# Performance work log

Hardware: AMD Instinct MI355X
Metric: run time of the kernel (lower is better)

Reference implementation:

```python
import jax, jax.numpy as jnp
import numpy as np

N, E, D, H, ED = 50000, 150000, 128, 4, 16


def _ln(x, g, b, eps=1e-5):
    m = jnp.mean(x, -1, keepdims=True)
    v = jnp.var(x, -1, keepdims=True)
    return (x - m) / jnp.sqrt(v + eps) * g + b


def _seg_softmax(logits, seg, n):
    # numerically stable softmax over edges grouped by destination node
    m = jax.ops.segment_max(logits, seg, num_segments=n)
    e = jnp.exp(logits - m[seg])
    s = jax.ops.segment_sum(e, seg, num_segments=n)
    return e / (s[seg] + 1e-16)


def setup_inputs():
    key = jax.random.key(0)
    ks = jax.random.split(key, 16)
    def w(i, shape, s=0.05):
        return jax.random.normal(ks[i], shape, jnp.float32) * s
    return dict(
        x=w(0, (N, D), 1.0),
        edge_index=jax.random.randint(ks[1], (2, E), 0, N),
        edge_attr=w(2, (E, ED), 1.0),
        sage_Wl=w(3, (D, D)), sage_Wr=w(4, (D, D)), sage_b=jnp.zeros((D,), jnp.float32),
        tq_W=w(5, (D, H * D)), tq_b=jnp.zeros((H * D,), jnp.float32),
        tk_W=w(6, (D, H * D)), tk_b=jnp.zeros((H * D,), jnp.float32),
        tv_W=w(7, (D, H * D)), tv_b=jnp.zeros((H * D,), jnp.float32),
        te_W=w(8, (ED, H * D)),
        tskip_W=w(9, (D, D)), tskip_b=jnp.zeros((D,), jnp.float32),
        gat_W=w(10, (D, H * D)), gat_att_src=w(11, (H, D)), gat_att_dst=w(12, (H, D)),
        gat_bias=jnp.zeros((D,), jnp.float32),
        gate_short=jnp.ones((1,), jnp.float32), gate_attn=jnp.ones((1,), jnp.float32),
        gate_neighbor=jnp.ones((1,), jnp.float32),
        fus_W=w(13, (3 * D, D)), fus_b=jnp.zeros((D,), jnp.float32),
        fus_g=jnp.ones((D,), jnp.float32), fus_beta=jnp.zeros((D,), jnp.float32),
        norm_g=jnp.ones((D,), jnp.float32), norm_b=jnp.zeros((D,), jnp.float32),
    )


def reference(x, edge_index, edge_attr, sage_Wl, sage_Wr, sage_b,
              tq_W, tq_b, tk_W, tk_b, tv_W, tv_b, te_W, tskip_W, tskip_b,
              gat_W, gat_att_src, gat_att_dst, gat_bias,
              gate_short, gate_attn, gate_neighbor,
              fus_W, fus_b, fus_g, fus_beta, norm_g, norm_b):
    n, d = x.shape
    h = tq_W.shape[1] // d
    src, dst = edge_index[0], edge_index[1]

    # --- SAGEConv: mean aggregation of neighbors + root linear ---
    agg = jax.ops.segment_sum(x[src], dst, num_segments=n)
    cnt = jax.ops.segment_sum(jnp.ones((src.shape[0],), x.dtype), dst, num_segments=n)
    mean = agg / jnp.maximum(cnt, 1.0)[:, None]
    x_short = jax.nn.relu(mean @ sage_Wl + x @ sage_Wr + sage_b)

    # --- TransformerConv (concat=False, edge-conditioned key/value, skip) ---
    q = (x @ tq_W + tq_b).reshape(n, h, d)
    k = (x @ tk_W + tk_b).reshape(n, h, d)
    v = (x @ tv_W + tv_b).reshape(n, h, d)
    e = (edge_attr @ te_W).reshape(-1, h, d)           # [E,H,d]
    logits = jnp.sum(q[dst] * (k[src] + e), -1) / np.float32(np.sqrt(d))  # [E,H]
    alpha = _seg_softmax(logits, dst, n)
    out_t = jax.ops.segment_sum((v[src] + e) * alpha[..., None], dst, num_segments=n).mean(1)
    x_attn = jax.nn.relu(out_t + x @ tskip_W + tskip_b)

    # --- GATConv (adds self-loops, concat=False averages heads, bias) ---
    loops = jnp.arange(n)
    s2 = jnp.concatenate([src, loops])
    d2 = jnp.concatenate([dst, loops])
    g = (x @ gat_W).reshape(n, h, d)
    a_s = jnp.sum(g * gat_att_src, -1)                 # [N,H]
    a_d = jnp.sum(g * gat_att_dst, -1)
    lg = jax.nn.leaky_relu(a_s[s2] + a_d[d2], 0.2)     # [E+N,H]
    al = _seg_softmax(lg, d2, n)
    out_g = jax.ops.segment_sum(g[s2] * al[..., None], d2, num_segments=n).mean(1) + gat_bias
    x_nb = jax.nn.relu(out_g)

    # --- gated fusion + residual LayerNorm ---
    gs = jax.nn.sigmoid(gate_short)
    ga = jax.nn.sigmoid(gate_attn)
    gn = jax.nn.sigmoid(gate_neighbor)
    cat = jnp.concatenate([x_short * gs, x_attn * ga, x_nb * gn], -1)
    fused = jax.nn.relu(_ln(cat @ fus_W + fus_b, fus_g, fus_beta))
    return _ln(x + fused, norm_g, norm_b)
```

## Files before the change

kernel.cpp:

```cpp
#include <hip/hip_runtime.h>
#include <hip/hip_bf16.h>

using bf16 = __hip_bfloat16;
typedef __attribute__((ext_vector_type(8))) short short8;
typedef __attribute__((ext_vector_type(4))) float f32x4;
typedef __attribute__((ext_vector_type(4))) unsigned short u16x4;

__device__ __forceinline__ void store4(bf16* p, float v0, float v1, float v2, float v3) {
    u16x4 pk;
    bf16 h0 = __float2bfloat16(v0); pk[0] = *(unsigned short*)&h0;
    bf16 h1 = __float2bfloat16(v1); pk[1] = *(unsigned short*)&h1;
    bf16 h2 = __float2bfloat16(v2); pk[2] = *(unsigned short*)&h2;
    bf16 h3 = __float2bfloat16(v3); pk[3] = *(unsigned short*)&h3;
    *(u16x4*)p = pk;
}
__device__ __forceinline__ float b2f(short s) { bf16 h; *(short*)&h = s; return __bfloat162float(h); }

__device__ __forceinline__ void ld_lds16(void* lds, const void* g) {
    __builtin_amdgcn_global_load_lds(
        (const __attribute__((address_space(1))) unsigned int*)g,
        (__attribute__((address_space(3))) unsigned int*)lds,
        16, 0, 0);
}

__device__ __forceinline__ size_t pidx(int c, int k, int K) {
    return ((size_t)(((c >> 6) * (K >> 5) + (k >> 5)) * 4 + ((c >> 4) & 3)) * 64
            + (((k >> 3) & 3) * 16 + (c & 15))) * 8 + (k & 7);
}

__global__ __launch_bounds__(256) void zero_ws(unsigned* p, size_t n) {
    size_t i = (size_t)blockIdx.x * 256 + threadIdx.x;
    size_t stride = (size_t)gridDim.x * 256;
    for (; i < n; i += stride) p[i] = 0u;
}

__global__ __launch_bounds__(256) void prep_all(
    const float* __restrict__ x, bf16* __restrict__ x_b,
    bf16* __restrict__ Wt_sage, const float* __restrict__ sage_Wl, const float* __restrict__ sage_Wr,
    bf16* __restrict__ Wt_fus, const float* __restrict__ fus_W,
    const float* __restrict__ gate_s, const float* __restrict__ gate_a, const float* __restrict__ gate_n,
    bf16* __restrict__ Wt_cat, const float* __restrict__ tvW,
    const float* __restrict__ tskipW, const float* __restrict__ teW,
    bf16* __restrict__ Wgag, const float* __restrict__ gatW,
    float* __restrict__ bvsum, const float* __restrict__ tvb, int ND)
{
    const int TP = 128 * 128;
    long i = (long)blockIdx.x * 256 + threadIdx.x;
    long nv = ND >> 3;
    if (i < nv) {
        long b = i * 8;
        f32x4 a0 = *(const f32x4*)(x + b);
        f32x4 a1 = *(const f32x4*)(x + b + 4);
        short8 o;
        #pragma unroll
        for (int j = 0; j < 4; ++j) { bf16 h = __float2bfloat16(a0[j]); o[j] = *(short*)&h; }
        #pragma unroll
        for (int j = 0; j < 4; ++j) { bf16 h = __float2bfloat16(a1[j]); o[4 + j] = *(short*)&h; }
        *(short8*)(x_b + b) = o;
        return;
    }
    i -= nv;
    if (i < TP) { int k = (int)i / 128, c = (int)i % 128; Wt_sage[pidx(c, k, 256)] = __float2bfloat16(sage_Wl[i]); return; }
    i -= TP;
    if (i < TP) { int k = (int)i / 128, c = (int)i % 128; Wt_sage[pidx(c, k + 128, 256)] = __float2bfloat16(sage_Wr[i]); return; }
    i -= TP;
    if (i < 3 * TP) {
        int sseg = (int)(i / TP); int r = (int)(i % TP);
        int k = r / 128, c = r % 128;
        const float* g = sseg == 0 ? gate_s : (sseg == 1 ? gate_a : gate_n);
        float gv = 1.0f / (1.0f + expf(-g[0]));
        Wt_fus[pidx(c, sseg * 128 + k, 384)] = __float2bfloat16(fus_W[(size_t)sseg * TP + r] * gv);
        return;
    }
    i -= 3L * TP;
    if (i < 128L * 704) {
        int d = (int)(i / 704), kk = (int)(i % 704);
        float v;
        if (kk < 512)      { int h = kk >> 7, k = kk & 127; v = 0.25f * tvW[k * 512 + h * 128 + d]; }
        else if (kk < 640) { int k = kk - 512;              v = tskipW[k * 128 + d]; }
        else               { int t = kk - 640; int h = t >> 4, j = t & 15; v = 0.25f * teW[j * 512 + h * 128 + d]; }
        Wt_cat[pidx(d, kk, 704)] = __float2bfloat16(v);
        return;
    }
    i -= 128L * 704;
    if (i < 128L * 512) {
        int d = (int)i >> 9, k = (int)i & 511;
        int h = k >> 7, i2 = k & 127;
        Wgag[pidx(d, k, 512)] = __float2bfloat16(0.25f * gatW[(size_t)i2 * 512 + h * 128 + d]);
        return;
    }
    i -= 128L * 512;
    if (i < 128) {
        int d = (int)i;
        bvsum[d] = 0.25f * (tvb[d] + tvb[128 + d] + tvb[256 + d] + tvb[384 + d]);
    }
}

__global__ __launch_bounds__(128) void build_wbig(
    bf16* __restrict__ Wbig, float* __restrict__ bbig,
    const float* __restrict__ Wq, const float* __restrict__ Wk,
    const float* __restrict__ teW, const float* __restrict__ bq,
    const float* __restrict__ bk, const float* __restrict__ gatW,
    const float* __restrict__ attS, const float* __restrict__ attD)
{
    int c = blockIdx.x;
    int ip = threadIdx.x;
    float acc = 0.f, bacc = 0.f;
    if (c < 512) {
        int h = c >> 7, i2 = c & 127;
        const float* wkrow = Wk + (size_t)i2 * 512 + h * 128;
        const float* wqrow = Wq + (size_t)ip * 512 + h * 128;
        for (int o = 0; o < 128; ++o) acc += wqrow[o] * wkrow[o];
        if (ip == 0) { const float* bqr = bq + h * 128; for (int o = 0; o < 128; ++o) bacc += bqr[o] * wkrow[o]; }
    } else if (c < 576) {
        int t = c - 512; int h = t >> 4, j = t & 15;
        const float* terow = teW + (size_t)j * 512 + h * 128;
        const float* wqrow = Wq + (size_t)ip * 512 + h * 128;
        for (int o = 0; o < 128; ++o) acc += wqrow[o] * terow[o];
        if (ip == 0) { const float* bqr = bq + h * 128; for (int o = 0; o < 128; ++o) bacc += bqr[o] * terow[o]; }
    } else if (c < 580) {
        int h = c - 576;
        const float* bkr = bk + h * 128;
        const float* wqrow = Wq + (size_t)ip * 512 + h * 128;
        for (int o = 0; o < 128; ++o) acc += wqrow[o] * bkr[o];
        if (ip == 0) { const float* bqr = bq + h * 128; for (int o = 0; o < 128; ++o) bacc += bqr[o] * bkr[o]; }
    } else if (c < 584) {
        int h = c - 580;
        const float* ar = attS + h * 128;
        const float* gr = gatW + (size_t)ip * 512 + h * 128;
        for (int d = 0; d < 128; ++d) acc += gr[d] * ar[d];
    } else if (c < 588) {
        int h = c - 584;
        const float* ar = attD + h * 128;
        const float* gr = gatW + (size_t)ip * 512 + h * 128;
        for (int d = 0; d < 128; ++d) acc += gr[d] * ar[d];
    }
    Wbig[pidx(c, ip, 128)] = __float2bfloat16(acc);
    if (ip == 0) bbig[c] = bacc;
}

__global__ __launch_bounds__(256) void k_hist(const int* __restrict__ dst, int* __restrict__ deg_i, int E) {
    int e = blockIdx.x * 256 + threadIdx.x;
    if (e < E) atomicAdd(&deg_i[dst[e]], 1);
}

__global__ __launch_bounds__(256) void k_scan1(
    const int* __restrict__ deg_i, int* __restrict__ loc, int* __restrict__ partial, int N)
{
    __shared__ int sm[256];
    int t = threadIdx.x, i = blockIdx.x * 256 + t;
    int v = (i < N) ? deg_i[i] : 0;
    sm[t] = v;
    __syncthreads();
    for (int off = 1; off < 256; off <<= 1) {
        int add = (t >= off) ? sm[t - off] : 0;
        __syncthreads();
        sm[t] += add;
        __syncthreads();
    }
    if (i < N) loc[i] = sm[t] - v;
    if (t == 255) partial[blockIdx.x] = sm[255];
}

__global__ __launch_bounds__(256) void k_scan2(int* __restrict__ partial, int nb) {
    __shared__ int sm[256];
    int t = threadIdx.x;
    int v = (t < nb) ? partial[t] : 0;
    sm[t] = v;
    __syncthreads();
    for (int off = 1; off < 256; off <<= 1) {
        int add = (t >= off) ? sm[t - off] : 0;
        __syncthreads();
        sm[t] += add;
        __syncthreads();
    }
    if (t < nb) partial[t] = sm[t] - v;
}

__global__ __launch_bounds__(256) void k_scan3(
    const int* __restrict__ loc, const int* __restrict__ partial,
    int* __restrict__ rowptr, int* __restrict__ cursor, int N)
{
    int i = blockIdx.x * 256 + threadIdx.x;
    if (i >= N) return;
    int r = loc[i] + partial[blockIdx.x];
    rowptr[i] = r;
    cursor[i] = r;
}

__global__ __launch_bounds__(256) void k_scatter(
    const int* __restrict__ src, const int* __restrict__ dst,
    int* __restrict__ cursor, int* __restrict__ col_src, int* __restrict__ eidx, int E)
{
    int e = blockIdx.x * 256 + threadIdx.x;
    if (e >= E) return;
    int d = dst[e];
    int pos = atomicAdd(&cursor[d], 1);
    col_src[pos] = src[e];
    eidx[pos] = e;
}

__global__ __launch_bounds__(128) void gemm_wide(
    const bf16* __restrict__ A, const bf16* __restrict__ Wt,
    const float* __restrict__ bias, bf16* __restrict__ C, int n_rows, int ldc)
{
    __shared__ __align__(16) short8 wstg[2][2][4][64];
    int row0 = blockIdx.x * 64;
    int wave = threadIdx.x >> 6, lane = threadIdx.x & 63;
    int lrow = lane & 15, quad = lane >> 4;
    short8 xb[4][4];
    #pragma unroll
    for (int ks = 0; ks < 4; ++ks)
        #pragma unroll
        for (int nt = 0; nt < 4; ++nt) {
            int r = row0 + nt * 16 + lrow;
            r = r < n_rows ? r : n_rows - 1;
            xb[ks][nt] = *(const short8*)(A + (size_t)r * 128 + ks * 32 + quad * 8);
        }
    auto issueW = [&](int c64, int ks, int par) {
        #pragma unroll
        for (int mt = 0; mt < 4; ++mt)
            ld_lds16(&wstg[wave][par][mt][0], Wt + ((size_t)((c64 * 4 + ks) * 4 + mt) * 64 + lane) * 8);
    };
    issueW(wave, 0, 0);
    int stp = 0;
    for (int cy = 0; cy < 5; ++cy) {
        int c64 = cy * 2 + wave;
        f32x4 acc[4][4] = {};
        #pragma unroll
        for (int ks = 0; ks < 4; ++ks) {
            int par = stp & 1;
            asm volatile("s_waitcnt vmcnt(0)" ::: "memory");
            int nst = stp + 1;
            if (nst < 20) issueW((nst >> 2) * 2 + wave, nst & 3, par ^ 1);
            short8 wf[4];
            #pragma unroll
            for (int mt = 0; mt < 4; ++mt) wf[mt] = wstg[wave][par][mt][lane];
            #pragma unroll
            for (int mt = 0; mt < 4; ++mt)
                #pragma unroll
                for (int nt = 0; nt < 4; ++nt)
                    acc[mt][nt] = __builtin_amdgcn_mfma_f32_16x16x32_bf16(wf[mt], xb[ks][nt], acc[mt][nt], 0, 0, 0);
            ++stp;
        }
        int cbase = c64 * 64;
        #pragma unroll
        for (int nt = 0; nt < 4; ++nt) {
            int row = row0 + nt * 16 + lrow;
            if (row >= n_rows) continue;
            #pragma unroll
            for (int mt = 0; mt < 4; ++mt) {
                int col = cbase + mt * 16 + quad * 4;
                float b0 = 0.f, b1 = 0.f, b2 = 0.f, b3 = 0.f;
                if (bias) { b0 = bias[col]; b1 = bias[col + 1]; b2 = bias[col + 2]; b3 = bias[col + 3]; }
                store4(&C[(size_t)row * ldc + col],
                       acc[mt][nt][0] + b0, acc[mt][nt][1] + b1,
                       acc[mt][nt][2] + b2, acc[mt][nt][3] + b3);
            }
        }
    }
}

#define NCAP 8
__global__ __launch_bounds__(256) void node_fused(
    const bf16* __restrict__ QT, const bf16* __restrict__ x_b,
    const float* __restrict__ edge_attr,
    const int* __restrict__ rowptr, const int* __restrict__ deg_i,
    const int* __restrict__ col_src, const int* __restrict__ eidx,
    bf16* __restrict__ mean_b, bf16* __restrict__ xa, bf16* __restrict__ ga,
    bf16* __restrict__ ea_b, int N)
{
    __shared__ short8 xS[4][NCAP][16];
    __shared__ float eaS[4][NCAP][16];
    __shared__ float wTs[4][NCAP][4];
    __shared__ float wGs[4][NCAP][4];
    int w = threadIdx.x >> 6, l = threadIdx.x & 63;
    int n = blockIdx.x * 4 + w;
    if (n >= N) return;
    int j = l & 15, g4 = l >> 4;
    int p0 = rowptr[n], dg = deg_i[n];
    const float scale = 0.08838834764831845f;
    float qtF[4][8], qeqL[4], qbL[4], adh[4], ashn[4];
    #pragma unroll
    for (int h = 0; h < 4; ++h) {
        short8 q = *(const short8*)(QT + (size_t)n * 640 + h * 128 + j * 8);
        #pragma unroll
        for (int t = 0; t < 8; ++t) qtF[h][t] = b2f(q[t]);
        qeqL[h] = __bfloat162float(QT[(size_t)n * 640 + 512 + h * 16 + j]);
        qbL[h]  = __bfloat162float(QT[(size_t)n * 640 + 576 + h]);
        ashn[h] = __bfloat162float(QT[(size_t)n * 640 + 580 + h]);
        adh[h]  = __bfloat162float(QT[(size_t)n * 640 + 584 + h]);
    }
    float xn0 = __bfloat162float(x_b[(size_t)n * 128 + l]);
    float xn1 = __bfloat162float(x_b[(size_t)n * 128 + l + 64]);
    float s_t[4], s_g[4], xaacc[8] = {}, gaacc[8];
    float mean0 = 0.f, mean1 = 0.f, eaacc = 0.f;
    #pragma unroll
    for (int h = 0; h < 4; ++h) {
        s_t[h] = 0.f;
        float lgs = ashn[h] + adh[h];
        lgs = lgs > 0.f ? lgs : 0.2f * lgs;
        float e = __expf(lgs);
        s_g[h] = e;
        gaacc[h * 2] = e * xn0; gaacc[h * 2 + 1] = e * xn1;
    }
    for (int c0 = 0; c0 < dg; c0 += NCAP) {
        int cc = min(NCAP, dg - c0);
        for (int it = 0; it < ((cc + 3) >> 2); ++it) {
            int i = it * 4 + g4;
            bool valid = i < cc;
            int s = 0;
            short8 xf = {0, 0, 0, 0, 0, 0, 0, 0};
            float ea_j = 0.f;
            if (valid) {
                s = col_src[p0 + c0 + i];
                int eg = eidx[p0 + c0 + i];
                xf = *(const short8*)(x_b + (size_t)s * 128 + j * 8);
                ea_j = edge_attr[(size_t)eg * 16 + j];
                xS[w][i][j] = xf;
                eaS[w][i][j] = ea_j;
            }
            float xv[8];
            #pragma unroll
            for (int t = 0; t < 8; ++t) xv[t] = b2f(xf[t]);
            float p[4];
            #pragma unroll
            for (int h = 0; h < 4; ++h) {
                float a = ea_j * qeqL[h];
                #pragma unroll
                for (int t = 0; t < 8; ++t) a += xv[t] * qtF[h][t];
                p[h] = a;
            }
            #pragma unroll
            for (int off = 1; off < 16; off <<= 1)
                #pragma unroll
                for (int h = 0; h < 4; ++h)
                    p[h] += __shfl_xor(p[h], off, 64);
            if (valid && j == 0) {
                #pragma unroll
                for (int h = 0; h < 4; ++h) {
                    wTs[w][i][h] = __expf((p[h] + qbL[h]) * scale);
                    float as_s = __bfloat162float(QT[(size_t)s * 640 + 580 + h]);
                    float lg = as_s + adh[h];
                    lg = lg > 0.f ? lg : 0.2f * lg;
                    wGs[w][i][h] = __expf(lg);
                }
            }
        }
        for (int i = 0; i < cc; ++i) {
            const bf16* xr = (const bf16*)&xS[w][i][0];
            float xv0 = __bfloat162float(xr[l]);
            float xv1 = __bfloat162float(xr[l + 64]);
            mean0 += xv0; mean1 += xv1;
            #pragma unroll
            for (int h = 0; h < 4; ++h) {
                float at = wTs[w][i][h], ag = wGs[w][i][h];
                s_t[h] += at; s_g[h] += ag;
                xaacc[h * 2] += at * xv0; xaacc[h * 2 + 1] += at * xv1;
                gaacc[h * 2] += ag * xv0; gaacc[h * 2 + 1] += ag * xv1;
            }
            eaacc += wTs[w][i][g4] * eaS[w][i][j];
        }
    }
    float invd = 1.f / fmaxf((float)dg, 1.f);
    mean_b[(size_t)n * 128 + l]      = __float2bfloat16(mean0 * invd);
    mean_b[(size_t)n * 128 + l + 64] = __float2bfloat16(mean1 * invd);
    #pragma unroll
    for (int h = 0; h < 4; ++h) {
        float it = 1.f / (s_t[h] + 1e-16f);
        xa[(size_t)n * 512 + h * 128 + l]      = __float2bfloat16(xaacc[h * 2] * it);
        xa[(size_t)n * 512 + h * 128 + l + 64] = __float2bfloat16(xaacc[h * 2 + 1] * it);
        float ig = 1.f / (s_g[h] + 1e-16f);
        ga[(size_t)n * 512 + h * 128 + l]      = __float2bfloat16(gaacc[h * 2] * ig);
        ga[(size_t)n * 512 + h * 128 + l + 64] = __float2bfloat16(gaacc[h * 2 + 1] * ig);
    }
    ea_b[(size_t)n * 64 + l] = __float2bfloat16(eaacc / (s_t[g4] + 1e-16f));
}

#define STASH(BIASP, USE_BV) do { \
    _Pragma("unroll") \
    for (int nt = 0; nt < 4; ++nt) { \
        int row_l = nt * 16 + lrow; \
        int sw = (row_l & 7) << 4; \
        float bvf = (USE_BV) ? ((deg_i[rA[nt]] > 0) ? 1.f : 0.f) : 0.f; \
        _Pragma("unroll") \
        for (int mt = 0; mt < 4; ++mt) { \
            int col = cbase + mt * 16 + quad * 4; \
            f32x4 bb = *(const f32x4*)((BIASP) + col); \
            u16x4 pk; \
            _Pragma("unroll") \
            for (int jj = 0; jj < 4; ++jj) { \
                float v = acc[mt][nt][jj] + bb[jj]; \
                if (USE_BV) v += bvf * bvsum[col + jj]; \
                bf16 h = __float2bfloat16(fmaxf(v, 0.f)); \
                pk[jj] = *(unsigned short*)&h; \
            } \
            *(u16x4*)(tileb + row_l * 256 + ((col * 2) ^ sw)) = pk; \
        } \
    } \
} while (0)

__global__ __launch_bounds__(128) void tail_fused(
    const bf16* __restrict__ mean_b, const bf16* __restrict__ x_b,
    const bf16* __restrict__ ga, const bf16* __restrict__ xa,
    const bf16* __restrict__ ea_b, const int* __restrict__ deg_i,
    const float* __restrict__ x,
    const bf16* __restrict__ Wt_sage, const bf16* __restrict__ Wgag,
    const bf16* __restrict__ Wt_cat, const bf16* __restrict__ Wt_fus,
    const float* __restrict__ sage_b, const float* __restrict__ gat_bias,
    const float* __restrict__ tskip_b, const float* __restrict__ bvsum,
    const float* __restrict__ fus_b, const float* __restrict__ fus_g,
    const float* __restrict__ fus_beta, const float* __restrict__ norm_g,
    const float* __restrict__ norm_b,
    float* __restrict__ out, int N)
{
    __shared__ __align__(16) char tileb[64 * 256];
    __shared__ __align__(16) short8 stg[2][2][8][64];
    __shared__ float2 st1[2][64];
    __shared__ float2 st2[2][64];
    int wave = threadIdx.x >> 6, lane = threadIdx.x & 63;
    int lrow = lane & 15, quad = lane >> 4;
    int kq = quad * 8;
    int row0 = blockIdx.x * 64;
    int cbase = wave * 64;
    int rA[4];
    #pragma unroll
    for (int t = 0; t < 4; ++t) {
        int r = row0 + t * 16 + lrow;
        rA[t] = r < N ? r : N - 1;
    }
    f32x4 facc[4][4] = {};

    auto issueA = [&](const bf16* base, int ldA, int kA, int par) {
        #pragma unroll
        for (int t = 0; t < 4; ++t)
            ld_lds16(&stg[wave][par][t][0], base + (size_t)rA[t] * ldA + kA);
    };
    auto issueW = [&](const bf16* Wt, int stepIdx, int par) {
        #pragma unroll
        for (int mt = 0; mt < 4; ++mt)
            ld_lds16(&stg[wave][par][4 + mt][0], Wt + ((size_t)(stepIdx * 4 + mt) * 64 + lane) * 8);
    };
    auto mfstep = [&](f32x4 (&acc)[4][4], int par) {
        short8 xf[4], wf[4];
        #pragma unroll
        for (int t = 0; t < 4; ++t) { xf[t] = stg[wave][par][t][lane]; wf[t] = stg[wave][par][4 + t][lane]; }
        #pragma unroll
        for (int mt = 0; mt < 4; ++mt)
            #pragma unroll
            for (int nt = 0; nt < 4; ++nt)
                acc[mt][nt] = __builtin_amdgcn_mfma_f32_16x16x32_bf16(wf[mt], xf[nt], acc[mt][nt], 0, 0, 0);
    };
    auto fuse_seg = [&](int SEG) {
        issueW(Wt_fus, wave * 12 + SEG * 4, 0);
        for (int ks = 0; ks < 4; ++ks) {
            int cur = ks & 1;
            asm volatile("s_waitcnt vmcnt(0)" ::: "memory");
            if (ks + 1 < 4) issueW(Wt_fus, wave * 12 + SEG * 4 + ks + 1, cur ^ 1);
            int kT = ks * 32 + kq;
            short8 xf[4], wf[4];
            #pragma unroll
            for (int t = 0; t < 4; ++t) {
                int row_l = t * 16 + lrow;
                xf[t] = *(const short8*)(tileb + row_l * 256 + ((kT * 2) ^ ((row_l & 7) << 4)));
            }
            #pragma unroll
            for (int mt = 0; mt < 4; ++mt) wf[mt] = stg[wave][cur][4 + mt][lane];
            #pragma unroll
            for (int mt = 0; mt < 4; ++mt)
                #pragma unroll
                for (int nt = 0; nt < 4; ++nt)
                    facc[mt][nt] = __builtin_amdgcn_mfma_f32_16x16x32_bf16(wf[mt], xf[nt], facc[mt][nt], 0, 0, 0);
        }
    };

    {
        f32x4 acc[4][4] = {};
        issueA(mean_b, 128, kq, 0);
        issueW(Wt_sage, wave * 8, 0);
        for (int ks = 0; ks < 8; ++ks) {
            int cur = ks & 1;
            asm volatile("s_waitcnt vmcnt(0)" ::: "memory");
            if (ks + 1 < 8) {
                int p = ks + 1;
                issueA((p < 4) ? mean_b : x_b, 128, (p & 3) * 32 + kq, cur ^ 1);
                issueW(Wt_sage, wave * 8 + p, cur ^ 1);
            }
            mfstep(acc, cur);
        }
        STASH(sage_b, 0);
    }
    __syncthreads();
    fuse_seg(0);
    __syncthreads();

    {
        f32x4 acc[4][4] = {};
        issueA(xa, 512, kq, 0);
        issueW(Wt_cat, wave * 22, 0);
        for (int ks = 0; ks < 22; ++ks) {
            int cur = ks & 1;
            asm volatile("s_waitcnt vmcnt(0)" ::: "memory");
            if (ks + 1 < 22) {
                int p = ks + 1;
                if (p < 16)      issueA(xa,   512, p * 32 + kq,        cur ^ 1);
                else if (p < 20) issueA(x_b,  128, (p - 16) * 32 + kq, cur ^ 1);
                else             issueA(ea_b,  64, (p - 20) * 32 + kq, cur ^ 1);
                issueW(Wt_cat, wave * 22 + p, cur ^ 1);
            }
            mfstep(acc, cur);
        }
        STASH(tskip_b, 1);
    }
    __syncthreads();
    fuse_seg(1);
    __syncthreads();

    {
        f32x4 acc[4][4] = {};
        issueA(ga, 512, kq, 0);
        issueW(Wgag, wave * 16, 0);
        for (int ks = 0; ks < 16; ++ks) {
            int cur = ks & 1;
            asm volatile("s_waitcnt vmcnt(0)" ::: "memory");
            if (ks + 1 < 16) {
                int p = ks + 1;
                issueA(ga, 512, p * 32 + kq, cur ^ 1);
                issueW(Wgag, wave * 16 + p, cur ^ 1);
            }
            mfstep(acc, cur);
        }
        STASH(gat_bias, 0);
    }
    __syncthreads();
    fuse_seg(2);

    #pragma unroll
    for (int nt = 0; nt < 4; ++nt) {
        float s = 0.f, q = 0.f;
        #pragma unroll
        for (int mt = 0; mt < 4; ++mt) {
            int col = cbase + mt * 16 + quad * 4;
            f32x4 bb = *(const f32x4*)(fus_b + col);
            #pragma unroll
            for (int jj = 0; jj < 4; ++jj) {
                float v = facc[mt][nt][jj] + bb[jj];
                facc[mt][nt][jj] = v;
                s += v; q += v * v;
            }
        }
        s += __shfl_xor(s, 16, 64); q += __shfl_xor(q, 16, 64);
        s += __shfl_xor(s, 32, 64); q += __shfl_xor(q, 32, 64);
        if (quad == 0) st1[wave][nt * 16 + lrow] = make_float2(s, q);
    }
    __syncthreads();
    float m1[4], inv1[4];
    #pragma unroll
    for (int nt = 0; nt < 4; ++nt) {
        float2 a = st1[0][nt * 16 + lrow], b = st1[1][nt * 16 + lrow];
        float S = a.x + b.x, Q = a.y + b.y;
        float m = S * (1.f / 128.f);
        m1[nt] = m;
        inv1[nt] = rsqrtf(Q * (1.f / 128.f) - m * m + 1e-5f);
    }
    #pragma unroll
    for (int nt = 0; nt < 4; ++nt) {
        float s = 0.f, q = 0.f;
        #pragma unroll
        for (int mt = 0; mt < 4; ++mt) {
            int col = cbase + mt * 16 + quad * 4;
            f32x4 gv = *(const f32x4*)(fus_g + col);
            f32x4 bv = *(const f32x4*)(fus_beta + col);
            f32x4 xv = *(const f32x4*)(x + (size_t)rA[nt] * 128 + col);
            #pragma unroll
            for (int jj = 0; jj < 4; ++jj) {
                float y = fmaxf((facc[mt][nt][jj] - m1[nt]) * inv1[nt] * gv[jj] + bv[jj], 0.f);
                float z = xv[jj] + y;
                facc[mt][nt][jj] = z;
                s += z; q += z * z;
            }
        }
        s += __shfl_xor(s, 16, 64); q += __shfl_xor(q, 16, 64);
        s += __shfl_xor(s, 32, 64); q += __shfl_xor(q, 32, 64);
        if (quad == 0) st2[wave][nt * 16 + lrow] = make_float2(s, q);
    }
    __syncthreads();
    #pragma unroll
    for (int nt = 0; nt < 4; ++nt) {
        int row = row0 + nt * 16 + lrow;
        if (row >= N) continue;
        float2 a = st2[0][nt * 16 + lrow], b = st2[1][nt * 16 + lrow];
        float S = a.x + b.x, Q = a.y + b.y;
        float m = S * (1.f / 128.f);
        float inv = rsqrtf(Q * (1.f / 128.f) - m * m + 1e-5f);
        #pragma unroll
        for (int mt = 0; mt < 4; ++mt) {
            int col = cbase + mt * 16 + quad * 4;
            f32x4 ngv = *(const f32x4*)(norm_g + col);
            f32x4 nbv = *(const f32x4*)(norm_b + col);
            f32x4 o;
            #pragma unroll
            for (int jj = 0; jj < 4; ++jj)
                o[jj] = (facc[mt][nt][jj] - m) * inv * ngv[jj] + nbv[jj];
            *(f32x4*)(out + (size_t)row * 128 + col) = o;
        }
    }
}

extern "C" void kernel_launch(void* const* d_in, const int* in_sizes, int n_in,
                              void* d_out, int out_size, void* d_ws, size_t ws_size,
                              hipStream_t stream)
{
    const float* x        = (const float*)d_in[0];
    const int*   ei       = (const int*)d_in[1];
    const float* edge_attr= (const float*)d_in[2];
    const float* sage_Wl  = (const float*)d_in[3];
    const float* sage_Wr  = (const float*)d_in[4];
    const float* sage_b   = (const float*)d_in[5];
    const float* tq_W     = (const float*)d_in[6];
    const float* tq_b     = (const float*)d_in[7];
    const float* tk_W     = (const float*)d_in[8];
    const float* tk_b     = (const float*)d_in[9];
    const float* tv_W     = (const float*)d_in[10];
    const float* tv_b     = (const float*)d_in[11];
    const float* te_W     = (const float*)d_in[12];
    const float* tskip_W  = (const float*)d_in[13];
    const float* tskip_b  = (const float*)d_in[14];
    const float* gat_W    = (const float*)d_in[15];
    const float* att_s_w  = (const float*)d_in[16];
    const float* att_d_w  = (const float*)d_in[17];
    const float* gat_bias = (const float*)d_in[18];
    const float* gate_s   = (const float*)d_in[19];
    const float* gate_a   = (const float*)d_in[20];
    const float* gate_n   = (const float*)d_in[21];
    const float* fus_W    = (const float*)d_in[22];
    const float* fus_b    = (const float*)d_in[23];
    const float* fus_g    = (const float*)d_in[24];
    const float* fus_beta = (const float*)d_in[25];
    const float* norm_g   = (const float*)d_in[26];
    const float* norm_b   = (const float*)d_in[27];

    int N = in_sizes[0] / 128;
    int E = in_sizes[2] / 16;
    const int* src = ei;
    const int* dst = ei + E;
    int ND = N * 128;
    int nb = (N + 255) / 256;

    char* wsb = (char*)d_ws;
    size_t off = 0;
    auto carve = [&](size_t bytes) -> char* {
        char* p = wsb + off;
        off += (bytes + 255) & ~(size_t)255;
        return p;
    };
    int*   deg_i   = (int*)carve((size_t)N * 4);
    size_t zero_bytes = off;
    int*   rowptr  = (int*)carve((size_t)N * 4);
    int*   cursor  = (int*)carve((size_t)N * 4);
    int*   loc     = (int*)carve((size_t)N * 4);
    int*   partial = (int*)carve((size_t)256 * 4);
    int*   col_src = (int*)carve((size_t)E * 4);
    int*   eidx    = (int*)carve((size_t)E * 4);
    bf16*  x_b     = (bf16*)carve((size_t)N * 128 * 2);
    bf16*  QT      = (bf16*)carve((size_t)N * 640 * 2);
    bf16*  xa      = (bf16*)carve((size_t)N * 512 * 2);
    bf16*  ga      = (bf16*)carve((size_t)N * 512 * 2);
    bf16*  mean_b  = (bf16*)carve((size_t)N * 128 * 2);
    bf16*  ea_b    = (bf16*)carve((size_t)N * 64 * 2);
    bf16*  Wbig    = (bf16*)carve((size_t)640 * 128 * 2);
    float* bbig    = (float*)carve((size_t)640 * 4);
    bf16*  Wt_sage = (bf16*)carve((size_t)128 * 256 * 2);
    bf16*  Wt_fus  = (bf16*)carve((size_t)128 * 384 * 2);
    bf16*  Wt_cat  = (bf16*)carve((size_t)128 * 704 * 2);
    bf16*  Wgag    = (bf16*)carve((size_t)128 * 512 * 2);
    float* bvsum   = (float*)carve((size_t)128 * 4);

    zero_ws<<<256, 256, 0, stream>>>((unsigned*)wsb, zero_bytes / 4);
    const long TP = 128 * 128;
    long prep_total = (long)(ND >> 3) + 5L * TP + 128L * 704 + 128L * 512 + 128;
    int prep_blocks = (int)((prep_total + 255) / 256);
    prep_all<<<prep_blocks, 256, 0, stream>>>(
        x, x_b, Wt_sage, sage_Wl, sage_Wr, Wt_fus, fus_W, gate_s, gate_a, gate_n,
        Wt_cat, tv_W, tskip_W, te_W, Wgag, gat_W, bvsum, tv_b, ND);
    build_wbig<<<640, 128, 0, stream>>>(Wbig, bbig, tq_W, tk_W, te_W, tq_b, tk_b,
                                        gat_W, att_s_w, att_d_w);

    k_hist<<<(E + 255) / 256, 256, 0, stream>>>(dst, deg_i, E);
    k_scan1<<<nb, 256, 0, stream>>>(deg_i, loc, partial, N);
    k_scan2<<<1, 256, 0, stream>>>(partial, nb);
    k_scan3<<<nb, 256, 0, stream>>>(loc, partial, rowptr, cursor, N);
    k_scatter<<<(E + 255) / 256, 256, 0, stream>>>(src, dst, cursor, col_src, eidx, E);

    int gy64 = (N + 63) / 64, gnode = (N + 3) / 4;

    gemm_wide<<<gy64, 128, 0, stream>>>(x_b, Wbig, bbig, QT, N, 640);

    node_fused<<<gnode, 256, 0, stream>>>(QT, x_b, edge_attr, rowptr, deg_i, col_src, eidx,
                                          mean_b, xa, ga, ea_b, N);

    tail_fused<<<gy64, 128, 0, stream>>>(
        mean_b, x_b, ga, xa, ea_b, deg_i, x,
        Wt_sage, Wgag, Wt_cat, Wt_fus,
        sage_b, gat_bias, tskip_b, bvsum,
        fus_b, fus_g, fus_beta, norm_g, norm_b,
        (float*)d_out, N);
}
```

Baseline: 371.5 us.

## Split wide GEMM over column grid and deepen tail GEMM prefetch pipeline

gemm_wide now launches a 2D grid where each block handles one 128-column slice and loads weights straight from global memory into registers, replacing the single block that looped over five column chunks through an LDS ring. This gives five times as many blocks for parallelism, but each block reloads its A rows. In tail_fused the LDS double-buffer prefetch now runs two stages ahead, waits on partial vmcnt instead of draining fully, and adds an lgkmcnt wait before a buffer is overwritten, so more memory latency overlaps the MFMA work. The hand-written vmcnt counts depend on exactly how many loads each issue produces, so any mismatch risks a data race.

```diff
diff --git a/kernel.cpp b/kernel.cpp
--- a/kernel.cpp
+++ b/kernel.cpp
@@ -204,7 +204,6 @@
     const bf16* __restrict__ A, const bf16* __restrict__ Wt,
     const float* __restrict__ bias, bf16* __restrict__ C, int n_rows, int ldc)
 {
-    __shared__ __align__(16) short8 wstg[2][2][4][64];
     int row0 = blockIdx.x * 64;
     int wave = threadIdx.x >> 6, lane = threadIdx.x & 63;
     int lrow = lane & 15, quad = lane >> 4;
@@ -217,46 +216,33 @@
             r = r < n_rows ? r : n_rows - 1;
             xb[ks][nt] = *(const short8*)(A + (size_t)r * 128 + ks * 32 + quad * 8);
         }
-    auto issueW = [&](int c64, int ks, int par) {
+    int c64 = blockIdx.y * 2 + wave;
+    int cbase = c64 * 64;
+    f32x4 acc[4][4] = {};
+    #pragma unroll
+    for (int ks = 0; ks < 4; ++ks) {
+        short8 wf[4];
         #pragma unroll
         for (int mt = 0; mt < 4; ++mt)
-            ld_lds16(&wstg[wave][par][mt][0], Wt + ((size_t)((c64 * 4 + ks) * 4 + mt) * 64 + lane) * 8);
-    };
-    issueW(wave, 0, 0);
-    int stp = 0;
-    for (int cy = 0; cy < 5; ++cy) {
-        int c64 = cy * 2 + wave;
-        f32x4 acc[4][4] = {};
-        #pragma unroll
-        for (int ks = 0; ks < 4; ++ks) {
-            int par = stp & 1;
-            asm volatile("s_waitcnt vmcnt(0)" ::: "memory");
-            int nst = stp + 1;
-            if (nst < 20) issueW((nst >> 2) * 2 + wave, nst & 3, par ^ 1);
-            short8 wf[4];
-            #pragma unroll
-            for (int mt = 0; mt < 4; ++mt) wf[mt] = wstg[wave][par][mt][lane];
-            #pragma unroll
-            for (int mt = 0; mt < 4; ++mt)
-                #pragma unroll
-                for (int nt = 0; nt < 4; ++nt)
-                    acc[mt][nt] = __builtin_amdgcn_mfma_f32_16x16x32_bf16(wf[mt], xb[ks][nt], acc[mt][nt], 0, 0, 0);
-            ++stp;
-        }
-        int cbase = c64 * 64;
-        #pragma unroll
-        for (int nt = 0; nt < 4; ++nt) {
-            int row = row0 + nt * 16 + lrow;
-            if (row >= n_rows) continue;
-            #pragma unroll
-            for (int mt = 0; mt < 4; ++mt) {
-                int col = cbase + mt * 16 + quad * 4;
-                float b0 = 0.f, b1 = 0.f, b2 = 0.f, b3 = 0.f;
-                if (bias) { b0 = bias[col]; b1 = bias[col + 1]; b2 = bias[col + 2]; b3 = bias[col + 3]; }
-                store4(&C[(size_t)row * ldc + col],
-                       acc[mt][nt][0] + b0, acc[mt][nt][1] + b1,
-                       acc[mt][nt][2] + b2, acc[mt][nt][3] + b3);
-            }
+            wf[mt] = *(const short8*)(Wt + ((size_t)((c64 * 4 + ks) * 4 + mt) * 64 + lane) * 8);
+        #pragma unroll
+        for (int mt = 0; mt < 4; ++mt)
+            #pragma unroll
+            for (int nt = 0; nt < 4; ++nt)
+                acc[mt][nt] = __builtin_amdgcn_mfma_f32_16x16x32_bf16(wf[mt], xb[ks][nt], acc[mt][nt], 0, 0, 0);
+    }
+    #pragma unroll
+    for (int nt = 0; nt < 4; ++nt) {
+        int row = row0 + nt * 16 + lrow;
+        if (row >= n_rows) continue;
+        #pragma unroll
+        for (int mt = 0; mt < 4; ++mt) {
+            int col = cbase + mt * 16 + quad * 4;
+            float b0 = 0.f, b1 = 0.f, b2 = 0.f, b3 = 0.f;
+            if (bias) { b0 = bias[col]; b1 = bias[col + 1]; b2 = bias[col + 2]; b3 = bias[col + 3]; }
+            store4(&C[(size_t)row * ldc + col],
+                   acc[mt][nt][0] + b0, acc[mt][nt][1] + b1,
+                   acc[mt][nt][2] + b2, acc[mt][nt][3] + b3);
         }
     }
 }
@@ -453,10 +439,12 @@
     };
     auto fuse_seg = [&](int SEG) {
         issueW(Wt_fus, wave * 12 + SEG * 4, 0);
+        issueW(Wt_fus, wave * 12 + SEG * 4 + 1, 1);
+        #pragma unroll
         for (int ks = 0; ks < 4; ++ks) {
             int cur = ks & 1;
-            asm volatile("s_waitcnt vmcnt(0)" ::: "memory");
-            if (ks + 1 < 4) issueW(Wt_fus, wave * 12 + SEG * 4 + ks + 1, cur ^ 1);
+            if (ks < 3) asm volatile("s_waitcnt vmcnt(4)" ::: "memory");
+            else        asm volatile("s_waitcnt vmcnt(0)" ::: "memory");
             int kT = ks * 32 + kq;
             short8 xf[4], wf[4];
             #pragma unroll
@@ -471,6 +459,10 @@
                 #pragma unroll
                 for (int nt = 0; nt < 4; ++nt)
                     facc[mt][nt] = __builtin_amdgcn_mfma_f32_16x16x32_bf16(wf[mt], xf[nt], facc[mt][nt], 0, 0, 0);
+            if (ks + 2 < 4) {
+                asm volatile("s_waitcnt lgkmcnt(0)" ::: "memory");
+                issueW(Wt_fus, wave * 12 + SEG * 4 + ks + 2, cur);
+            }
         }
     };
 
@@ -478,15 +470,20 @@
         f32x4 acc[4][4] = {};
         issueA(mean_b, 128, kq, 0);
         issueW(Wt_sage, wave * 8, 0);
+        issueA(mean_b, 128, 32 + kq, 1);
+        issueW(Wt_sage, wave * 8 + 1, 1);
+        #pragma unroll
         for (int ks = 0; ks < 8; ++ks) {
             int cur = ks & 1;
-            asm volatile("s_waitcnt vmcnt(0)" ::: "memory");
-            if (ks + 1 < 8) {
-                int p = ks + 1;
-                issueA((p < 4) ? mean_b : x_b, 128, (p & 3) * 32 + kq, cur ^ 1);
-                issueW(Wt_sage, wave * 8 + p, cur ^ 1);
-            }
+            if (ks < 7) asm volatile("s_waitcnt vmcnt(8)" ::: "memory");
+            else        asm volatile("s_waitcnt vmcnt(0)" ::: "memory");
             mfstep(acc, cur);
+            if (ks + 2 < 8) {
+                asm volatile("s_waitcnt lgkmcnt(0)" ::: "memory");
+                int p = ks + 2;
+                issueA((p < 4) ? mean_b : x_b, 128, (p & 3) * 32 + kq, cur);
+                issueW(Wt_sage, wave * 8 + p, cur);
+            }
         }
         STASH(sage_b, 0);
     }
@@ -498,17 +495,22 @@
         f32x4 acc[4][4] = {};
         issueA(xa, 512, kq, 0);
         issueW(Wt_cat, wave * 22, 0);
+        issueA(xa, 512, 32 + kq, 1);
+        issueW(Wt_cat, wave * 22 + 1, 1);
+        #pragma unroll
         for (int ks = 0; ks < 22; ++ks) {
             int cur = ks & 1;
-            asm volatile("s_waitcnt vmcnt(0)" ::: "memory");
-            if (ks + 1 < 22) {
-                int p = ks + 1;
-                if (p < 16)      issueA(xa,   512, p * 32 + kq,        cur ^ 1);
-                else if (p < 20) issueA(x_b,  128, (p - 16) * 32 + kq, cur ^ 1);
-                else             issueA(ea_b,  64, (p - 20) * 32 + kq, cur ^ 1);
-                issueW(Wt_cat, wave * 22 + p, cur ^ 1);
-            }
+            if (ks < 21) asm volatile("s_waitcnt vmcnt(8)" ::: "memory");
+            else         asm volatile("s_waitcnt vmcnt(0)" ::: "memory");
             mfstep(acc, cur);
+            if (ks + 2 < 22) {
+                asm volatile("s_waitcnt lgkmcnt(0)" ::: "memory");
+                int p = ks + 2;
+                if (p < 16)      issueA(xa,   512, p * 32 + kq,        cur);
+                else if (p < 20) issueA(x_b,  128, (p - 16) * 32 + kq, cur);
+                else             issueA(ea_b,  64, (p - 20) * 32 + kq, cur);
+                issueW(Wt_cat, wave * 22 + p, cur);
+            }
         }
         STASH(tskip_b, 1);
     }
@@ -520,15 +522,20 @@
         f32x4 acc[4][4] = {};
         issueA(ga, 512, kq, 0);
         issueW(Wgag, wave * 16, 0);
+        issueA(ga, 512, 32 + kq, 1);
+        issueW(Wgag, wave * 16 + 1, 1);
+        #pragma unroll
         for (int ks = 0; ks < 16; ++ks) {
             int cur = ks & 1;
-            asm volatile("s_waitcnt vmcnt(0)" ::: "memory");
-            if (ks + 1 < 16) {
-                int p = ks + 1;
-                issueA(ga, 512, p * 32 + kq, cur ^ 1);
-                issueW(Wgag, wave * 16 + p, cur ^ 1);
-            }
+            if (ks < 15) asm volatile("s_waitcnt vmcnt(8)" ::: "memory");
+            else         asm volatile("s_waitcnt vmcnt(0)" ::: "memory");
             mfstep(acc, cur);
+            if (ks + 2 < 16) {
+                asm volatile("s_waitcnt lgkmcnt(0)" ::: "memory");
+                int p = ks + 2;
+                issueA(ga, 512, p * 32 + kq, cur);
+                issueW(Wgag, wave * 16 + p, cur);
+            }
         }
         STASH(gat_bias, 0);
     }
@@ -694,7 +701,7 @@
 
     int gy64 = (N + 63) / 64, gnode = (N + 3) / 4;
 
-    gemm_wide<<<gy64, 128, 0, stream>>>(x_b, Wbig, bbig, QT, N, 640);
+    gemm_wide<<<dim3(gy64, 5), 128, 0, stream>>>(x_b, Wbig, bbig, QT, N, 640);
 
     node_fused<<<gnode, 256, 0, stream>>>(QT, x_b, edge_attr, rowptr, deg_i, col_src, eidx,
                                           mean_b, xa, ga, ea_b, N);
```

Measured after the change: 373.4 us. Within noise of the previous version (+0.5%).
